# Performance work log

Hardware: AMD Instinct MI355X
Metric: run time of the kernel (lower is better)

Reference implementation:

```python
import jax, jax.numpy as jnp
import numpy as np

B, S, H, D = 2, 2048, 16, 64
HID = H * D
NEG_INF = -10000.0

def setup_inputs() -> dict:
    key = jax.random.key(0)
    ks = jax.random.split(key, 4)
    std = 0.02
    return {
        'x': jax.random.normal(ks[0], (B, S, HID), dtype=jnp.float32),
        'mask': jnp.ones((B, S), dtype=jnp.int32),
        'Wq': jax.random.normal(ks[1], (HID, HID), dtype=jnp.float32) * std,
        'bq': jnp.zeros((HID,), dtype=jnp.float32),
        'Wk': jax.random.normal(ks[2], (HID, HID), dtype=jnp.float32) * std,
        'bk': jnp.zeros((HID,), dtype=jnp.float32),
        'Wv': jax.random.normal(ks[3], (HID, HID), dtype=jnp.float32) * std,
        'bv': jnp.zeros((HID,), dtype=jnp.float32),
    }

def reference(x, mask, Wq, bq, Wk, bk, Wv, bv):
    b, s, _ = x.shape
    def split_heads(t):  # [b,s,HID] -> [b,H,s,D]
        return t.reshape(b, s, H, D).transpose(0, 2, 1, 3)
    q = split_heads(x @ Wq + bq)
    k = split_heads(x @ Wk + bk)
    v = split_heads(x @ Wv + bv)
    scores = jnp.einsum('bhqd,bhkd->bhqk', q, k) / jnp.sqrt(jnp.float32(D))
    # additive padding mask: [b,1,1,s] broadcast over query positions and heads
    adder = (1.0 - mask.astype(scores.dtype))[:, None, None, :] * NEG_INF
    probs = jax.nn.softmax(scores + adder, axis=-1)
    ctx = jnp.einsum('bhqk,bhkd->bhqd', probs, v)  # [b,H,s,D]
    return ctx.transpose(0, 2, 1, 3).reshape(b, s, HID)
```

## Files before the change

kernel.cpp:

```cpp
#include <hip/hip_runtime.h>
#include <cstddef>

constexpr int Bc = 2, Sc = 2048, Hc = 16, Dc = 64, HIDc = 1024;
#define NEG_INF -10000.0f
#define LOG2E 1.44269504088896340736f

typedef _Float16 half8  __attribute__((ext_vector_type(8)));
typedef _Float16 half4  __attribute__((ext_vector_type(4)));
typedef float   floatx4 __attribute__((ext_vector_type(4)));

__global__ __launch_bounds__(256) void cvt_x_kernel(const float* __restrict__ x,
                                                    _Float16* __restrict__ xh) {
    int i = (blockIdx.x * 256 + threadIdx.x) * 8;
    float4 a = *(const float4*)(x + i);
    float4 b = *(const float4*)(x + i + 4);
    half8 h;
    h[0] = (_Float16)a.x; h[1] = (_Float16)a.y; h[2] = (_Float16)a.z; h[3] = (_Float16)a.w;
    h[4] = (_Float16)b.x; h[5] = (_Float16)b.y; h[6] = (_Float16)b.z; h[7] = (_Float16)b.w;
    *(half8*)(xh + i) = h;
}

__global__ __launch_bounds__(256) void cvt_w_kernel(const float* __restrict__ Wq,
                                                    const float* __restrict__ Wk,
                                                    const float* __restrict__ Wv,
                                                    _Float16* __restrict__ Wt) {
    const float* W = (blockIdx.z == 0) ? Wq : (blockIdx.z == 1) ? Wk : Wv;
    _Float16* out = Wt + (size_t)blockIdx.z * HIDc * HIDc;
    __shared__ _Float16 T[64][65];
    const int t = threadIdx.x;
    const int kb = blockIdx.x * 64, nb = blockIdx.y * 64;
    const int r = t >> 2, c4 = (t & 3) * 16;
    #pragma unroll
    for (int i = 0; i < 16; i += 4) {
        float4 a = *(const float4*)(W + (size_t)(kb + r) * HIDc + nb + c4 + i);
        T[c4 + i + 0][r] = (_Float16)a.x;
        T[c4 + i + 1][r] = (_Float16)a.y;
        T[c4 + i + 2][r] = (_Float16)a.z;
        T[c4 + i + 3][r] = (_Float16)a.w;
    }
    __syncthreads();
    const int n = t >> 2, k4 = (t & 3) * 16;
    half8 o0, o1;
    #pragma unroll
    for (int j = 0; j < 8; ++j) { o0[j] = T[n][k4 + j]; o1[j] = T[n][k4 + 8 + j]; }
    *(half8*)(out + (size_t)(nb + n) * HIDc + kb + k4)     = o0;
    *(half8*)(out + (size_t)(nb + n) * HIDc + kb + k4 + 8) = o1;
}

#define PSTR 40
__global__ __launch_bounds__(256, 2) void proj_kernel(
    const _Float16* __restrict__ xh, const _Float16* __restrict__ Wt,
    const float* __restrict__ bq, const float* __restrict__ bk, const float* __restrict__ bv,
    _Float16* __restrict__ qw, _Float16* __restrict__ kw, _Float16* __restrict__ vt)
{
    const int z = blockIdx.z;
    const _Float16* Wz = Wt + (size_t)z * HIDc * HIDc;
    const float* bias = (z == 0) ? bq : (z == 1) ? bk : bv;

    __shared__ __align__(16) _Float16 SM[4][128 * PSTR];

    const int t = threadIdx.x;
    const int lane = t & 63, w = t >> 6;
    const int quad = lane >> 4, l16 = lane & 15;
    const int m0 = blockIdx.y * 128, n0 = blockIdx.x * 128;
    const int wm = (w >> 1) * 64, wn = (w & 1) * 64;
    const int sr = t >> 1, sh = (t & 1) * 16;

    floatx4 acc[4][4];
    #pragma unroll
    for (int mb = 0; mb < 4; ++mb)
        #pragma unroll
        for (int nb = 0; nb < 4; ++nb) acc[mb][nb] = floatx4{0.f, 0.f, 0.f, 0.f};

    {
        const _Float16* ap = xh + (size_t)(m0 + sr) * HIDc + sh;
        const _Float16* bp = Wz + (size_t)(n0 + sr) * HIDc + sh;
        *(uint4*)(SM[0] + sr * PSTR + sh)     = *(const uint4*)(ap);
        *(uint4*)(SM[0] + sr * PSTR + sh + 8) = *(const uint4*)(ap + 8);
        *(uint4*)(SM[2] + sr * PSTR + sh)     = *(const uint4*)(bp);
        *(uint4*)(SM[2] + sr * PSTR + sh + 8) = *(const uint4*)(bp + 8);
    }
    __syncthreads();

    #pragma unroll 2
    for (int it = 0; it < HIDc / 32; ++it) {
        const int cur = it & 1;
        const int kn = (it + 1 < HIDc / 32) ? (it + 1) * 32 : 0;
        const _Float16* ap = xh + (size_t)(m0 + sr) * HIDc + kn + sh;
        const _Float16* bp = Wz + (size_t)(n0 + sr) * HIDc + kn + sh;
        uint4 a0 = *(const uint4*)(ap);
        uint4 a1 = *(const uint4*)(ap + 8);
        uint4 b0 = *(const uint4*)(bp);
        uint4 b1 = *(const uint4*)(bp + 8);

        half8 af[4], bf[4];
        #pragma unroll
        for (int mb = 0; mb < 4; ++mb)
            af[mb] = *(const half8*)(SM[cur] + (wm + mb * 16 + l16) * PSTR + quad * 8);
        #pragma unroll
        for (int nb = 0; nb < 4; ++nb)
            bf[nb] = *(const half8*)(SM[2 + cur] + (wn + nb * 16 + l16) * PSTR + quad * 8);
        #pragma unroll
        for (int mb = 0; mb < 4; ++mb)
            #pragma unroll
            for (int nb = 0; nb < 4; ++nb)
                acc[mb][nb] = __builtin_amdgcn_mfma_f32_16x16x32_f16(
                    af[mb], bf[nb], acc[mb][nb], 0, 0, 0);

        *(uint4*)(SM[cur ^ 1] + sr * PSTR + sh)           = a0;
        *(uint4*)(SM[cur ^ 1] + sr * PSTR + sh + 8)       = a1;
        *(uint4*)(SM[2 + (cur ^ 1)] + sr * PSTR + sh)     = b0;
        *(uint4*)(SM[2 + (cur ^ 1)] + sr * PSTR + sh + 8) = b1;
        __syncthreads();
    }

    if (z == 2) {
        _Float16* T = &SM[0][0];
        #pragma unroll
        for (int nb = 0; nb < 4; ++nb) {
            const int n = wn + nb * 16 + l16;
            const float bi = bias[n0 + n];
            #pragma unroll
            for (int mb = 0; mb < 4; ++mb) {
                half4 h4;
                #pragma unroll
                for (int r = 0; r < 4; ++r) h4[r] = (_Float16)(acc[mb][nb][r] + bi);
                *(half4*)(T + n * 136 + wm + mb * 16 + quad * 4) = h4;
            }
        }
        __syncthreads();
        const int bI0 = m0 >> 11, m0s = m0 & (Sc - 1);
        #pragma unroll
        for (int p = 0; p < 2; ++p) {
            const int n = p * 64 + (t >> 2);
            const int N = n0 + n, hh = N >> 6, d = N & 63;
            _Float16* vrow = vt + (((size_t)(bI0 * Hc + hh)) * Dc + d) * Sc + m0s;
            #pragma unroll
            for (int j = 0; j < 4; ++j) {
                const int c = (t & 3) * 32 + j * 8;
                *(uint4*)(vrow + c) = *(const uint4*)(T + n * 136 + c);
            }
        }
        return;
    }
    #pragma unroll
    for (int nb = 0; nb < 4; ++nb) {
        const int N = n0 + wn + nb * 16 + l16;
        const float bi = bias[N];
        const int h = N >> 6, d = N & 63;
        #pragma unroll
        for (int mb = 0; mb < 4; ++mb) {
            #pragma unroll
            for (int r = 0; r < 4; ++r) {
                const int M = m0 + wm + mb * 16 + quad * 4 + r;
                const int bI = M >> 11, s = M & (Sc - 1);
                const float v = acc[mb][nb][r] + bi;
                if (z == 0)
                    qw[(((size_t)(bI * Hc + h)) * Sc + s) * Dc + d] =
                        (_Float16)(v * (0.125f * LOG2E));
                else
                    kw[(((size_t)(bI * Hc + h)) * Sc + s) * Dc + d] = (_Float16)v;
            }
        }
    }
}

__global__ __launch_bounds__(256, 2) void attn_kernel(
    const _Float16* __restrict__ qw, const _Float16* __restrict__ kw,
    const _Float16* __restrict__ vt, const int* __restrict__ mask,
    float* __restrict__ out)
{
    __shared__ __align__(16) float adder[Sc];
    __shared__ __align__(16) _Float16 Ks[2][64][72];
    __shared__ __align__(16) _Float16 Vs[2][64][72];

    const int t = threadIdx.x;
    const int lane = t & 63, w = t >> 6;
    const int quad = lane >> 4, l16 = lane & 15;
    const int bh = blockIdx.y;
    const int bI = bh >> 4, h = bh & 15;

    const _Float16* Qp = qw + (size_t)bh * Sc * Dc;
    const _Float16* Kp = kw + (size_t)bh * Sc * Dc;
    const _Float16* Vp = vt + (size_t)bh * Dc * Sc;

    const int srow = t >> 3;
    const int scol = (t & 7) * 8;
    const int m7 = t & 7;
    const int vc0 = 32 * (m7 & 1) + 4 * (m7 >> 1);

    {
        const int4* mp = (const int4*)(mask + bI * Sc);
        #pragma unroll
        for (int i = 0; i < 2; ++i) {
            int4 m4 = mp[t * 2 + i];
            int base = (t * 2 + i) * 4;
            adder[base + 0] = (1.0f - (float)m4.x) * (NEG_INF * LOG2E);
            adder[base + 1] = (1.0f - (float)m4.y) * (NEG_INF * LOG2E);
            adder[base + 2] = (1.0f - (float)m4.z) * (NEG_INF * LOG2E);
            adder[base + 3] = (1.0f - (float)m4.w) * (NEG_INF * LOG2E);
        }
    }
    #pragma unroll
    for (int hf = 0; hf < 2; ++hf) {
        const int row = srow + 32 * hf;
        uint4 kv = *(const uint4*)(Kp + (size_t)row * Dc + scol);
        uint4 vv = *(const uint4*)(Vp + (size_t)row * Sc + scol);
        *(uint4*)(&Ks[0][row][scol]) = kv;
        *(uint2*)(&Vs[0][row][vc0])      = make_uint2(vv.x, vv.y);
        *(uint2*)(&Vs[0][row][vc0 + 16]) = make_uint2(vv.z, vv.w);
    }

    const int qrow = blockIdx.x * 128 + w * 32;
    half8 aq[2][2];
    #pragma unroll
    for (int s = 0; s < 2; ++s)
        #pragma unroll
        for (int hh = 0; hh < 2; ++hh)
            aq[s][hh] = *(const half8*)(Qp + (size_t)(qrow + 16 * s + l16) * Dc
                                        + hh * 32 + quad * 8);

    floatx4 o[2][4], osum[2];
    #pragma unroll
    for (int s = 0; s < 2; ++s) {
        osum[s] = floatx4{0.f, 0.f, 0.f, 0.f};
        #pragma unroll
        for (int db = 0; db < 4; ++db) o[s][db] = floatx4{0.f, 0.f, 0.f, 0.f};
    }
    const half4 ones4 = {(_Float16)1.f, (_Float16)1.f, (_Float16)1.f, (_Float16)1.f};

    __syncthreads();

    #pragma unroll 2
    for (int it = 0; it < Sc / 64; ++it) {
        const int cur = it & 1;
        const int kt = it * 64;
        const int ktn = (it + 1 < Sc / 64) ? kt + 64 : 0;
        uint4 kstg[2], vstg[2];
        #pragma unroll
        for (int hf = 0; hf < 2; ++hf) {
            const int row = srow + 32 * hf;
            kstg[hf] = *(const uint4*)(Kp + (size_t)(ktn + row) * Dc + scol);
            vstg[hf] = *(const uint4*)(Vp + (size_t)row * Sc + ktn + scol);
        }

        half8 kb[4][2];
        #pragma unroll
        for (int nb = 0; nb < 4; ++nb)
            #pragma unroll
            for (int hh = 0; hh < 2; ++hh)
                kb[nb][hh] = *(const half8*)(&Ks[cur][nb * 16 + l16][hh * 32 + quad * 8]);

        half4 vb[4][4];
        #pragma unroll
        for (int db = 0; db < 4; ++db)
            #pragma unroll
            for (int hf2 = 0; hf2 < 2; ++hf2) {
                const half8 v8 = *(const half8*)(&Vs[cur][db * 16 + l16][quad * 16 + hf2 * 8]);
                vb[hf2 * 2 + 0][db] = __builtin_shufflevector(v8, v8, 0, 1, 2, 3);
                vb[hf2 * 2 + 1][db] = __builtin_shufflevector(v8, v8, 4, 5, 6, 7);
            }

        floatx4 st[2][4];
        __builtin_amdgcn_s_setprio(1);
        #pragma unroll
        for (int nb = 0; nb < 4; ++nb) {
            const floatx4 adv = *(const floatx4*)(&adder[kt + nb * 16 + quad * 4]);
            #pragma unroll
            for (int s = 0; s < 2; ++s) {
                floatx4 x0 = __builtin_amdgcn_mfma_f32_16x16x32_f16(kb[nb][0], aq[s][0], adv, 0, 0, 0);
                st[s][nb]  = __builtin_amdgcn_mfma_f32_16x16x32_f16(kb[nb][1], aq[s][1], x0, 0, 0, 0);
            }
        }
        __builtin_amdgcn_s_setprio(0);

        half4 pa[2][4];
        #pragma unroll
        for (int s = 0; s < 2; ++s)
            #pragma unroll
            for (int nb = 0; nb < 4; ++nb)
                #pragma unroll
                for (int r = 0; r < 4; ++r)
                    pa[s][nb][r] = (_Float16)__builtin_amdgcn_exp2f(st[s][nb][r]);

        __builtin_amdgcn_s_setprio(1);
        #pragma unroll
        for (int s = 0; s < 2; ++s)
            #pragma unroll
            for (int nb = 0; nb < 4; ++nb) {
                osum[s] = __builtin_amdgcn_mfma_f32_16x16x16f16(pa[s][nb], ones4, osum[s], 0, 0, 0);
                #pragma unroll
                for (int db = 0; db < 4; ++db)
                    o[s][db] = __builtin_amdgcn_mfma_f32_16x16x16f16(
                        pa[s][nb], vb[nb][db], o[s][db], 0, 0, 0);
            }
        __builtin_amdgcn_s_setprio(0);

        #pragma unroll
        for (int hf = 0; hf < 2; ++hf) {
            const int row = srow + 32 * hf;
            *(uint4*)(&Ks[cur ^ 1][row][scol]) = kstg[hf];
            const uint4 vv = vstg[hf];
            *(uint2*)(&Vs[cur ^ 1][row][vc0])      = make_uint2(vv.x, vv.y);
            *(uint2*)(&Vs[cur ^ 1][row][vc0 + 16]) = make_uint2(vv.z, vv.w);
        }
        __syncthreads();
    }

    float* op = out + (size_t)bI * Sc * HIDc + h * Dc;
    #pragma unroll
    for (int s = 0; s < 2; ++s)
        #pragma unroll
        for (int r = 0; r < 4; ++r) {
            const float inv = __builtin_amdgcn_rcpf(osum[s][r]);
            const int q = qrow + 16 * s + quad * 4 + r;
            #pragma unroll
            for (int db = 0; db < 4; ++db)
                op[(size_t)q * HIDc + db * 16 + l16] = o[s][db][r] * inv;
        }
}

extern "C" void kernel_launch(void* const* d_in, const int* in_sizes, int n_in,
                              void* d_out, int out_size, void* d_ws, size_t ws_size,
                              hipStream_t stream) {
    const float* x    = (const float*)d_in[0];
    const int*   mask = (const int*)  d_in[1];
    const float* Wq   = (const float*)d_in[2];
    const float* bq   = (const float*)d_in[3];
    const float* Wk   = (const float*)d_in[4];
    const float* bk   = (const float*)d_in[5];
    const float* Wv   = (const float*)d_in[6];
    const float* bv   = (const float*)d_in[7];
    float* out = (float*)d_out;

    char* ws = (char*)d_ws;
    _Float16* xh = (_Float16*)(ws);
    _Float16* Wt = (_Float16*)(ws + (size_t)8  * 1024 * 1024);
    _Float16* qw = (_Float16*)(ws + (size_t)14 * 1024 * 1024);
    _Float16* kw = (_Float16*)(ws + (size_t)22 * 1024 * 1024);
    _Float16* vt = (_Float16*)(ws + (size_t)30 * 1024 * 1024);

    cvt_x_kernel<<<(Bc * Sc * HIDc) / (256 * 8), 256, 0, stream>>>(x, xh);
    cvt_w_kernel<<<dim3(HIDc / 64, HIDc / 64, 3), 256, 0, stream>>>(Wq, Wk, Wv, Wt);
    proj_kernel<<<dim3(HIDc / 128, (Bc * Sc) / 128, 3), 256, 0, stream>>>(
        xh, Wt, bq, bk, bv, qw, kw, vt);
    attn_kernel<<<dim3(Sc / 128, Bc * Hc), 256, 0, stream>>>(qw, kw, vt, mask, out);
}
```

Before: 179.2 us.

## Stage projection GEMM tiles with direct global-to-LDS loads and XOR swizzle

The QKV projection GEMM now copies A and B tiles straight from global memory into LDS with global_load_lds, replacing the register round-trip and explicit LDS stores. The padded LDS layout is dropped in favour of an unpadded 32-wide row with an XOR swizzle to avoid bank conflicts. This shrinks shared memory, which allows launch bounds of three blocks per SM. The V transpose epilogue is split into two passes so it fits the smaller LDS buffer, at the cost of extra barriers.

```diff
diff --git a/kernel.cpp b/kernel.cpp
--- a/kernel.cpp
+++ b/kernel.cpp
@@ -8,6 +8,12 @@
 typedef _Float16 half8  __attribute__((ext_vector_type(8)));
 typedef _Float16 half4  __attribute__((ext_vector_type(4)));
 typedef float   floatx4 __attribute__((ext_vector_type(4)));
+
+__device__ __forceinline__ void gload_lds16(const void* g, void* l) {
+    __builtin_amdgcn_global_load_lds(
+        (const __attribute__((address_space(1))) unsigned int*)g,
+        (__attribute__((address_space(3))) unsigned int*)l, 16, 0, 0);
+}
 
 __global__ __launch_bounds__(256) void cvt_x_kernel(const float* __restrict__ x,
                                                     _Float16* __restrict__ xh) {
@@ -47,8 +53,7 @@
     *(half8*)(out + (size_t)(nb + n) * HIDc + kb + k4 + 8) = o1;
 }
 
-#define PSTR 40
-__global__ __launch_bounds__(256, 2) void proj_kernel(
+__global__ __launch_bounds__(256, 3) void proj_kernel(
     const _Float16* __restrict__ xh, const _Float16* __restrict__ Wt,
     const float* __restrict__ bq, const float* __restrict__ bk, const float* __restrict__ bv,
     _Float16* __restrict__ qw, _Float16* __restrict__ kw, _Float16* __restrict__ vt)
@@ -57,14 +62,16 @@
     const _Float16* Wz = Wt + (size_t)z * HIDc * HIDc;
     const float* bias = (z == 0) ? bq : (z == 1) ? bk : bv;
 
-    __shared__ __align__(16) _Float16 SM[4][128 * PSTR];
+    __shared__ __align__(16) _Float16 SM[2][2][128 * 32];
 
     const int t = threadIdx.x;
     const int lane = t & 63, w = t >> 6;
     const int quad = lane >> 4, l16 = lane & 15;
     const int m0 = blockIdx.y * 128, n0 = blockIdx.x * 128;
     const int wm = (w >> 1) * 64, wn = (w & 1) * 64;
-    const int sr = t >> 1, sh = (t & 1) * 16;
+
+    const int srl = lane >> 2;
+    const int ssl = (lane & 3) ^ ((lane >> 3) & 3);
 
     floatx4 acc[4][4];
     #pragma unroll
@@ -72,68 +79,68 @@
         #pragma unroll
         for (int nb = 0; nb < 4; ++nb) acc[mb][nb] = floatx4{0.f, 0.f, 0.f, 0.f};
 
-    {
-        const _Float16* ap = xh + (size_t)(m0 + sr) * HIDc + sh;
-        const _Float16* bp = Wz + (size_t)(n0 + sr) * HIDc + sh;
-        *(uint4*)(SM[0] + sr * PSTR + sh)     = *(const uint4*)(ap);
-        *(uint4*)(SM[0] + sr * PSTR + sh + 8) = *(const uint4*)(ap + 8);
-        *(uint4*)(SM[2] + sr * PSTR + sh)     = *(const uint4*)(bp);
-        *(uint4*)(SM[2] + sr * PSTR + sh + 8) = *(const uint4*)(bp + 8);
-    }
+    auto stage = [&](int buf, int kt) {
+        #pragma unroll
+        for (int j = 0; j < 2; ++j) {
+            const int rb = (w + 4 * j) * 16;
+            gload_lds16(xh + (size_t)(m0 + rb + srl) * HIDc + kt + ssl * 8,
+                        &SM[buf][0][rb * 32]);
+            gload_lds16(Wz + (size_t)(n0 + rb + srl) * HIDc + kt + ssl * 8,
+                        &SM[buf][1][rb * 32]);
+        }
+    };
+
+    stage(0, 0);
     __syncthreads();
+
+    const int sA = (quad ^ ((l16 >> 1) & 3)) * 8;
 
     #pragma unroll 2
     for (int it = 0; it < HIDc / 32; ++it) {
         const int cur = it & 1;
         const int kn = (it + 1 < HIDc / 32) ? (it + 1) * 32 : 0;
-        const _Float16* ap = xh + (size_t)(m0 + sr) * HIDc + kn + sh;
-        const _Float16* bp = Wz + (size_t)(n0 + sr) * HIDc + kn + sh;
-        uint4 a0 = *(const uint4*)(ap);
-        uint4 a1 = *(const uint4*)(ap + 8);
-        uint4 b0 = *(const uint4*)(bp);
-        uint4 b1 = *(const uint4*)(bp + 8);
+        stage(cur ^ 1, kn);
 
         half8 af[4], bf[4];
         #pragma unroll
         for (int mb = 0; mb < 4; ++mb)
-            af[mb] = *(const half8*)(SM[cur] + (wm + mb * 16 + l16) * PSTR + quad * 8);
+            af[mb] = *(const half8*)(&SM[cur][0][(wm + mb * 16 + l16) * 32 + sA]);
         #pragma unroll
         for (int nb = 0; nb < 4; ++nb)
-            bf[nb] = *(const half8*)(SM[2 + cur] + (wn + nb * 16 + l16) * PSTR + quad * 8);
+            bf[nb] = *(const half8*)(&SM[cur][1][(wn + nb * 16 + l16) * 32 + sA]);
         #pragma unroll
         for (int mb = 0; mb < 4; ++mb)
             #pragma unroll
             for (int nb = 0; nb < 4; ++nb)
                 acc[mb][nb] = __builtin_amdgcn_mfma_f32_16x16x32_f16(
                     af[mb], bf[nb], acc[mb][nb], 0, 0, 0);
-
-        *(uint4*)(SM[cur ^ 1] + sr * PSTR + sh)           = a0;
-        *(uint4*)(SM[cur ^ 1] + sr * PSTR + sh + 8)       = a1;
-        *(uint4*)(SM[2 + (cur ^ 1)] + sr * PSTR + sh)     = b0;
-        *(uint4*)(SM[2 + (cur ^ 1)] + sr * PSTR + sh + 8) = b1;
         __syncthreads();
     }
 
     if (z == 2) {
-        _Float16* T = &SM[0][0];
-        #pragma unroll
-        for (int nb = 0; nb < 4; ++nb) {
-            const int n = wn + nb * 16 + l16;
-            const float bi = bias[n0 + n];
-            #pragma unroll
-            for (int mb = 0; mb < 4; ++mb) {
-                half4 h4;
+        _Float16* T = (_Float16*)SM;
+        const int bI0 = m0 >> 11, m0s = m0 & (Sc - 1);
+        #pragma unroll
+        for (int p = 0; p < 2; ++p) {
+            __syncthreads();
+            if ((w & 1) == p) {
                 #pragma unroll
-                for (int r = 0; r < 4; ++r) h4[r] = (_Float16)(acc[mb][nb][r] + bi);
-                *(half4*)(T + n * 136 + wm + mb * 16 + quad * 4) = h4;
-            }
-        }
-        __syncthreads();
-        const int bI0 = m0 >> 11, m0s = m0 & (Sc - 1);
-        #pragma unroll
-        for (int p = 0; p < 2; ++p) {
-            const int n = p * 64 + (t >> 2);
-            const int N = n0 + n, hh = N >> 6, d = N & 63;
+                for (int nb = 0; nb < 4; ++nb) {
+                    const int n = nb * 16 + l16;
+                    const float bi = bias[n0 + p * 64 + n];
+                    #pragma unroll
+                    for (int mb = 0; mb < 4; ++mb) {
+                        half4 h4;
+                        #pragma unroll
+                        for (int r = 0; r < 4; ++r)
+                            h4[r] = (_Float16)(acc[mb][nb][r] + bi);
+                        *(half4*)(T + n * 136 + wm + mb * 16 + quad * 4) = h4;
+                    }
+                }
+            }
+            __syncthreads();
+            const int n = t >> 2;
+            const int N = n0 + p * 64 + n, hh = N >> 6, d = N & 63;
             _Float16* vrow = vt + (((size_t)(bI0 * Hc + hh)) * Dc + d) * Sc + m0s;
             #pragma unroll
             for (int j = 0; j < 4; ++j) {
```

Measured after the change: 168.5 us. 6.0% less time.
